# Optimization experiments

Hardware: AMD Instinct MI355X
Metric: run time of the kernel (lower is better)

## Reference

```python
import jax, jax.numpy as jnp
import numpy as np

N_NODES = 100000
N_EDGES = 1600000
IN_F = 256
OUT_F = 64


def setup_inputs() -> dict:
    key = jax.random.key(0)
    k1, k2, k3, k4, k5, k6 = jax.random.split(key, 6)
    x = jax.random.normal(k1, (N_NODES, IN_F), dtype=jnp.float32)
    edge_vals = jax.random.uniform(k2, (N_EDGES,), dtype=jnp.float32)
    W = jax.random.normal(k3, (IN_F, OUT_F), dtype=jnp.float32) * (1.0 / np.sqrt(OUT_F))
    bias = jax.random.normal(k4, (OUT_F,), dtype=jnp.float32) * (1.0 / np.sqrt(OUT_F))
    row_idx = jnp.sort(jax.random.randint(k5, (N_EDGES,), 0, N_NODES, dtype=jnp.int32))
    col_idx = jax.random.randint(k6, (N_EDGES,), 0, N_NODES, dtype=jnp.int32)
    return {"x": x, "edge_vals": edge_vals, "W": W, "bias": bias,
            "row_idx": row_idx, "col_idx": col_idx}


def reference(x, edge_vals, W, bias, row_idx, col_idx):
    # support = X @ W  (dense GEMM; torch.mm / torch.spmm branch)
    support = x @ W                                  # [N, OUT_F]
    # flexspmm: output = A @ support, A given as weighted edge list
    msgs = support[col_idx] * edge_vals[:, None]      # [E, OUT_F] gather + scale
    out = jax.ops.segment_sum(msgs, row_idx, num_segments=x.shape[0])  # [N, OUT_F]
    return out + bias
```

## Files before the change

### kernel.cpp

```cpp
#include <hip/hip_runtime.h>
#include <hip/hip_bf16.h>
#include <hip/hip_fp16.h>

#define N_NODES 100000
#define N_EDGES 1600000
#define IN_F 256
#define OUT_F 64

typedef short bf16x8 __attribute__((ext_vector_type(8)));
typedef float f32x4 __attribute__((ext_vector_type(4)));
typedef _Float16 half8 __attribute__((ext_vector_type(8)));

__device__ __forceinline__ short f2bf(float f) {
  unsigned u = __float_as_uint(f);
  u += 0x7FFF + ((u >> 16) & 1);
  return (short)(u >> 16);
}

__global__ __launch_bounds__(256) void prep_kernel(
    const int* __restrict__ row_idx, int* __restrict__ row_ptr,
    const float* __restrict__ W, short* __restrict__ Wf) {
  const int b = blockIdx.x;
  if (b < 392) {
    int i = b * 256 + threadIdx.x;
    if (i > N_NODES) return;
    int lo = 0, hi = N_EDGES;
    while (lo < hi) {
      int mid = (lo + hi) >> 1;
      if (row_idx[mid] < i) lo = mid + 1; else hi = mid;
    }
    row_ptr[i] = lo;
  } else {
    int tid = (b - 392) * 256 + threadIdx.x;
    int s = tid >> 8;
    int r = tid & 255;
    int t = r >> 6;
    int lane = r & 63;
    int col = t * 16 + (lane & 15);
    int kbase = s * 32 + ((lane >> 4) & 3) * 8;
#pragma unroll
    for (int j = 0; j < 8; ++j) {
      Wf[(size_t)tid * 8 + j] = f2bf(W[(size_t)(kbase + j) * OUT_F + col]);
    }
  }
}

__global__ __launch_bounds__(256) void gemm_kernel(
    const float* __restrict__ x, const short* __restrict__ Wf,
    _Float16* __restrict__ supH) {
  __shared__ short sWf[8 * 4 * 64 * 8];
  {
    const float4* g = reinterpret_cast<const float4*>(Wf);
    float4* s4 = reinterpret_cast<float4*>(sWf);
#pragma unroll
    for (int i = 0; i < 8; ++i) s4[threadIdx.x + i * 256] = g[threadIdx.x + i * 256];
  }
  __syncthreads();

  const int lane = threadIdx.x & 63;
  const int wave = threadIdx.x >> 6;
  const int r0_base = blockIdx.x * 64 + wave * 16;

  int arow = r0_base + (lane & 15);
  if (arow >= N_NODES) arow = N_NODES - 1;
  const float* xrow = x + (size_t)arow * IN_F + ((lane >> 4) & 3) * 8;

  f32x4 acc0 = {0.f, 0.f, 0.f, 0.f};
  f32x4 acc1 = {0.f, 0.f, 0.f, 0.f};
  f32x4 acc2 = {0.f, 0.f, 0.f, 0.f};
  f32x4 acc3 = {0.f, 0.f, 0.f, 0.f};

#pragma unroll
  for (int s = 0; s < 8; ++s) {
    const float4 f0 = *reinterpret_cast<const float4*>(xrow + s * 32);
    const float4 f1 = *reinterpret_cast<const float4*>(xrow + s * 32 + 4);
    bf16x8 a;
    a[0] = f2bf(f0.x); a[1] = f2bf(f0.y); a[2] = f2bf(f0.z); a[3] = f2bf(f0.w);
    a[4] = f2bf(f1.x); a[5] = f2bf(f1.y); a[6] = f2bf(f1.z); a[7] = f2bf(f1.w);
    const bf16x8 b0 = *reinterpret_cast<const bf16x8*>(&sWf[((s * 4 + 0) * 64 + lane) * 8]);
    const bf16x8 b1 = *reinterpret_cast<const bf16x8*>(&sWf[((s * 4 + 1) * 64 + lane) * 8]);
    const bf16x8 b2 = *reinterpret_cast<const bf16x8*>(&sWf[((s * 4 + 2) * 64 + lane) * 8]);
    const bf16x8 b3 = *reinterpret_cast<const bf16x8*>(&sWf[((s * 4 + 3) * 64 + lane) * 8]);
    acc0 = __builtin_amdgcn_mfma_f32_16x16x32_bf16(a, b0, acc0, 0, 0, 0);
    acc1 = __builtin_amdgcn_mfma_f32_16x16x32_bf16(a, b1, acc1, 0, 0, 0);
    acc2 = __builtin_amdgcn_mfma_f32_16x16x32_bf16(a, b2, acc2, 0, 0, 0);
    acc3 = __builtin_amdgcn_mfma_f32_16x16x32_bf16(a, b3, acc3, 0, 0, 0);
  }

  const int orow_base = r0_base + ((lane >> 4) & 3) * 4;
  const int ocol = lane & 15;
#pragma unroll
  for (int r = 0; r < 4; ++r) {
    const int row = orow_base + r;
    if (row < N_NODES) {
      _Float16* o = supH + (size_t)row * OUT_F + ocol;
      o[0]  = (_Float16)acc0[r];
      o[16] = (_Float16)acc1[r];
      o[32] = (_Float16)acc2[r];
      o[48] = (_Float16)acc3[r];
    }
  }
}

__global__ __launch_bounds__(256) void spmm_kernel(
    const _Float16* __restrict__ supH, const float* __restrict__ ev,
    const int* __restrict__ col, const int* __restrict__ row_ptr,
    const int* __restrict__ row_idx,
    const float* __restrict__ bias, float* __restrict__ out) {
  const int lane = threadIdx.x & 63;
  const int g = lane >> 3;
  const int fo = lane & 7;
  const int gwave = (blockIdx.x * blockDim.x + threadIdx.x) >> 6;
  const int nwaves = (gridDim.x * blockDim.x) >> 6;

  const long k0 = ((long)gwave * N_EDGES) / nwaves;
  const long k1 = ((long)(gwave + 1) * N_EDGES) / nwaves;
  const int n0 = (k0 == 0) ? 0 : (row_idx[k0 - 1] + 1);
  const int n1 = (gwave + 1 >= nwaves) ? N_NODES : (row_idx[k1 - 1] + 1);
  if (n0 >= n1) return;

  float b[8];
#pragma unroll
  for (int j = 0; j < 8; ++j) b[j] = bias[fo * 8 + j];

  int n = n0;
  int i = row_ptr[n0];
  int eCur = row_ptr[n0 + 1];
  int eNext = row_ptr[(n0 + 2 <= N_NODES) ? n0 + 2 : N_NODES];

  int pos0 = i + g, pos1 = i + 8 + g;
  int cp0 = pos0 < N_EDGES ? pos0 : N_EDGES - 1;
  int cp1 = pos1 < N_EDGES ? pos1 : N_EDGES - 1;
  int   c0 = col[cp0];
  int   c1 = col[cp1];
  float v0 = ev[cp0];
  float v1 = ev[cp1];

  float acc[8] = {0.f, 0.f, 0.f, 0.f, 0.f, 0.f, 0.f, 0.f};

  while (true) {
    const bool more = (i + 16 < eCur);
    const int ni = more ? (i + 16) : eCur;

    const int np0 = ni + g, np1 = ni + 8 + g;
    const int ncp0 = np0 < N_EDGES ? np0 : N_EDGES - 1;
    const int ncp1 = np1 < N_EDGES ? np1 : N_EDGES - 1;
    const int   nc0 = col[ncp0];
    const int   nc1 = col[ncp1];
    const float nv0 = ev[ncp0];
    const float nv1 = ev[ncp1];

    const float u0 = (pos0 < eCur) ? v0 : 0.f;
    const float u1 = (pos1 < eCur) ? v1 : 0.f;
    const half8 s0 = *reinterpret_cast<const half8*>(
        supH + (unsigned)((c0 << 6) + fo * 8));
    const half8 s1 = *reinterpret_cast<const half8*>(
        supH + (unsigned)((c1 << 6) + fo * 8));
#pragma unroll
    for (int j = 0; j < 8; ++j) acc[j] = fmaf(u0, (float)s0[j], acc[j]);
#pragma unroll
    for (int j = 0; j < 8; ++j) acc[j] = fmaf(u1, (float)s1[j], acc[j]);

    if (!more) {
#pragma unroll
      for (int j = 0; j < 8; ++j) {
        acc[j] += __shfl_xor(acc[j], 8);
        acc[j] += __shfl_xor(acc[j], 16);
        acc[j] += __shfl_xor(acc[j], 32);
      }
      if (lane < 8) {
        float* o = out + (size_t)n * OUT_F + fo * 8;
        f32x4 oA = {acc[0] + b[0], acc[1] + b[1], acc[2] + b[2], acc[3] + b[3]};
        f32x4 oB = {acc[4] + b[4], acc[5] + b[5], acc[6] + b[6], acc[7] + b[7]};
        *reinterpret_cast<f32x4*>(o) = oA;
        *reinterpret_cast<f32x4*>(o + 4) = oB;
      }
      ++n;
      if (n >= n1) break;
#pragma unroll
      for (int j = 0; j < 8; ++j) acc[j] = 0.f;
      eCur = eNext;
      eNext = row_ptr[(n + 2 <= N_NODES) ? n + 2 : N_NODES];
    }

    i = ni;
    pos0 = np0; pos1 = np1;
    c0 = nc0; c1 = nc1;
    v0 = nv0; v1 = nv1;
  }
}

extern "C" void kernel_launch(void* const* d_in, const int* in_sizes, int n_in,
                              void* d_out, int out_size, void* d_ws, size_t ws_size,
                              hipStream_t stream) {
  const float* x        = (const float*)d_in[0];
  const float* ev       = (const float*)d_in[1];
  const float* W        = (const float*)d_in[2];
  const float* bias     = (const float*)d_in[3];
  const int*   row_idx  = (const int*)d_in[4];
  const int*   col_idx  = (const int*)d_in[5];
  float* out = (float*)d_out;

  int*       row_ptr = (int*)d_ws;
  short*     Wf      = (short*)((char*)d_ws + 448 * 1024);
  _Float16*  supH    = (_Float16*)((char*)d_ws + 512 * 1024);

  prep_kernel<<<400, 256, 0, stream>>>(row_idx, row_ptr, W, Wf);

  gemm_kernel<<<(N_NODES + 63) / 64, 256, 0, stream>>>(x, Wf, supH);

  spmm_kernel<<<2048, 256, 0, stream>>>(supH, ev, col_idx, row_ptr, row_idx, bias, out);
}
```

Before: 69.26 us.

## Split support matrix into two feature halves and run SpMM twice

The GEMM now writes the fp16 support matrix as two planar halves of 32 features each, and the SpMM runs as two launches, one per half. Each half-table is 6.4MB instead of 12.8MB, so each pass's gather working set is more likely to stay in L2/LLC and cut DRAM traffic from random row gathers. In exchange, the col/ev/row_ptr index streams are read twice, and each wave now handles 16 edges per iteration with 4 lanes per edge, which adds one shuffle stage to the reduction.

Result: slower. 118.2 us (+70.7%).

```diff
diff --git a/kernel.cpp b/kernel.cpp
--- a/kernel.cpp
+++ b/kernel.cpp
@@ -47,7 +47,7 @@
 
 __global__ __launch_bounds__(256) void gemm_kernel(
     const float* __restrict__ x, const short* __restrict__ Wf,
-    _Float16* __restrict__ supH) {
+    _Float16* __restrict__ supP) {
   __shared__ short sWf[8 * 4 * 64 * 8];
   {
     const float4* g = reinterpret_cast<const float4*>(Wf);
@@ -93,23 +93,26 @@
   for (int r = 0; r < 4; ++r) {
     const int row = orow_base + r;
     if (row < N_NODES) {
-      _Float16* o = supH + (size_t)row * OUT_F + ocol;
-      o[0]  = (_Float16)acc0[r];
-      o[16] = (_Float16)acc1[r];
-      o[32] = (_Float16)acc2[r];
-      o[48] = (_Float16)acc3[r];
-    }
-  }
-}
-
-__global__ __launch_bounds__(256) void spmm_kernel(
-    const _Float16* __restrict__ supH, const float* __restrict__ ev,
+      _Float16* o0 = supP + (size_t)row * 32 + ocol;
+      _Float16* o1 = supP + (size_t)N_NODES * 32 + (size_t)row * 32 + ocol;
+      o0[0]  = (_Float16)acc0[r];
+      o0[16] = (_Float16)acc1[r];
+      o1[0]  = (_Float16)acc2[r];
+      o1[16] = (_Float16)acc3[r];
+    }
+  }
+}
+
+__global__ __launch_bounds__(256) void spmm_half_kernel(
+    const _Float16* __restrict__ supP,
+    const float* __restrict__ ev,
     const int* __restrict__ col, const int* __restrict__ row_ptr,
     const int* __restrict__ row_idx,
-    const float* __restrict__ bias, float* __restrict__ out) {
+    const float* __restrict__ biasHalf,
+    float* __restrict__ outHalf) {
   const int lane = threadIdx.x & 63;
-  const int g = lane >> 3;
-  const int fo = lane & 7;
+  const int g = lane >> 2;
+  const int fo = lane & 3;
   const int gwave = (blockIdx.x * blockDim.x + threadIdx.x) >> 6;
   const int nwaves = (gridDim.x * blockDim.x) >> 6;
 
@@ -121,20 +124,17 @@
 
   float b[8];
 #pragma unroll
-  for (int j = 0; j < 8; ++j) b[j] = bias[fo * 8 + j];
+  for (int j = 0; j < 8; ++j) b[j] = biasHalf[fo * 8 + j];
 
   int n = n0;
   int i = row_ptr[n0];
   int eCur = row_ptr[n0 + 1];
   int eNext = row_ptr[(n0 + 2 <= N_NODES) ? n0 + 2 : N_NODES];
 
-  int pos0 = i + g, pos1 = i + 8 + g;
-  int cp0 = pos0 < N_EDGES ? pos0 : N_EDGES - 1;
-  int cp1 = pos1 < N_EDGES ? pos1 : N_EDGES - 1;
-  int   c0 = col[cp0];
-  int   c1 = col[cp1];
-  float v0 = ev[cp0];
-  float v1 = ev[cp1];
+  int pos = i + g;
+  int cp = pos < N_EDGES ? pos : N_EDGES - 1;
+  int   c = col[cp];
+  float v = ev[cp];
 
   float acc[8] = {0.f, 0.f, 0.f, 0.f, 0.f, 0.f, 0.f, 0.f};
 
@@ -142,34 +142,27 @@
     const bool more = (i + 16 < eCur);
     const int ni = more ? (i + 16) : eCur;
 
-    const int np0 = ni + g, np1 = ni + 8 + g;
-    const int ncp0 = np0 < N_EDGES ? np0 : N_EDGES - 1;
-    const int ncp1 = np1 < N_EDGES ? np1 : N_EDGES - 1;
-    const int   nc0 = col[ncp0];
-    const int   nc1 = col[ncp1];
-    const float nv0 = ev[ncp0];
-    const float nv1 = ev[ncp1];
-
-    const float u0 = (pos0 < eCur) ? v0 : 0.f;
-    const float u1 = (pos1 < eCur) ? v1 : 0.f;
-    const half8 s0 = *reinterpret_cast<const half8*>(
-        supH + (unsigned)((c0 << 6) + fo * 8));
-    const half8 s1 = *reinterpret_cast<const half8*>(
-        supH + (unsigned)((c1 << 6) + fo * 8));
-#pragma unroll
-    for (int j = 0; j < 8; ++j) acc[j] = fmaf(u0, (float)s0[j], acc[j]);
-#pragma unroll
-    for (int j = 0; j < 8; ++j) acc[j] = fmaf(u1, (float)s1[j], acc[j]);
+    const int np = ni + g;
+    const int ncp = np < N_EDGES ? np : N_EDGES - 1;
+    const int   nc = col[ncp];
+    const float nv = ev[ncp];
+
+    const float u = (pos < eCur) ? v : 0.f;
+    const half8 s = *reinterpret_cast<const half8*>(
+        supP + (unsigned)((c << 5) + fo * 8));
+#pragma unroll
+    for (int j = 0; j < 8; ++j) acc[j] = fmaf(u, (float)s[j], acc[j]);
 
     if (!more) {
 #pragma unroll
       for (int j = 0; j < 8; ++j) {
+        acc[j] += __shfl_xor(acc[j], 4);
         acc[j] += __shfl_xor(acc[j], 8);
         acc[j] += __shfl_xor(acc[j], 16);
         acc[j] += __shfl_xor(acc[j], 32);
       }
-      if (lane < 8) {
-        float* o = out + (size_t)n * OUT_F + fo * 8;
+      if (lane < 4) {
+        float* o = outHalf + (size_t)n * OUT_F + fo * 8;
         f32x4 oA = {acc[0] + b[0], acc[1] + b[1], acc[2] + b[2], acc[3] + b[3]};
         f32x4 oB = {acc[4] + b[4], acc[5] + b[5], acc[6] + b[6], acc[7] + b[7]};
         *reinterpret_cast<f32x4*>(o) = oA;
@@ -184,9 +177,9 @@
     }
 
     i = ni;
-    pos0 = np0; pos1 = np1;
-    c0 = nc0; c1 = nc1;
-    v0 = nv0; v1 = nv1;
+    pos = np;
+    c = nc;
+    v = nv;
   }
 }
 
@@ -203,11 +196,15 @@
 
   int*       row_ptr = (int*)d_ws;
   short*     Wf      = (short*)((char*)d_ws + 448 * 1024);
-  _Float16*  supH    = (_Float16*)((char*)d_ws + 512 * 1024);
+  _Float16*  supP    = (_Float16*)((char*)d_ws + 512 * 1024);
 
   prep_kernel<<<400, 256, 0, stream>>>(row_idx, row_ptr, W, Wf);
 
-  gemm_kernel<<<(N_NODES + 63) / 64, 256, 0, stream>>>(x, Wf, supH);
-
-  spmm_kernel<<<2048, 256, 0, stream>>>(supH, ev, col_idx, row_ptr, row_idx, bias, out);
-}
+  gemm_kernel<<<(N_NODES + 63) / 64, 256, 0, stream>>>(x, Wf, supP);
+
+  spmm_half_kernel<<<2048, 256, 0, stream>>>(
+      supP, ev, col_idx, row_ptr, row_idx, bias, out);
+  spmm_half_kernel<<<2048, 256, 0, stream>>>(
+      supP + (size_t)N_NODES * 32, ev, col_idx, row_ptr, row_idx,
+      bias + 32, out + 32);
+}
```
